# Kernel tuning notes

Hardware: AMD Instinct MI355X
Metric: run time of the kernel (lower is better)

## Reference

```python
import jax, jax.numpy as jnp
import numpy as np

ALPHA = 1.0
BETA = 0.25
NUM_EMBEDS = 8192
EMBED_DIM = 512
B, T = 32, 256


def setup_inputs() -> dict:
    key = jax.random.key(0)
    k1, k2 = jax.random.split(key)
    z_e = jax.random.normal(k1, (B, EMBED_DIM, T), dtype=jnp.float32)
    codebook = jax.random.normal(k2, (NUM_EMBEDS, EMBED_DIM), dtype=jnp.float32)
    return {"z_e": z_e, "codebook": codebook}


def reference(z_e, codebook):
    # z_e: (b, d, t) -> (b, t, d)
    z = jnp.transpose(z_e, (0, 2, 1))
    b, t, d = z.shape
    flat = z.reshape(-1, d)  # (N, d), N = b*t

    # squared euclidean distances to every codebook vector: (N, K)
    dists = (
        jnp.sum(flat * flat, axis=1, keepdims=True)
        + jnp.sum(codebook * codebook, axis=1)
        - 2.0 * flat @ codebook.T
    )
    idx = jnp.argmin(dists, axis=1)  # (N,)

    # codebook lookup (equivalent to one-hot @ codebook)
    z_q = codebook[idx].reshape(b, t, d)

    # commitment loss (codebook is EMA-updated, so only e_latent term)
    e_latent_loss = jnp.mean((jax.lax.stop_gradient(z_q) - z) ** 2)
    vq_loss = ALPHA * BETA * e_latent_loss

    # straight-through estimator
    z_q_st = z + jax.lax.stop_gradient(z_q - z)
    z_q_out = jnp.transpose(z_q_st, (0, 2, 1))  # back to (b, d, t)

    # perplexity from mean one-hot assignment probabilities
    counts = jnp.zeros((codebook.shape[0],), dtype=jnp.float32).at[idx].add(1.0)
    avg_probs = counts / flat.shape[0]
    perplexity = jnp.exp(-jnp.sum(avg_probs * jnp.log(avg_probs + 1e-10)))

    return z_q_out, vq_loss, perplexity
```

## Files before the change

kernel.cpp:

```cpp
#include <hip/hip_runtime.h>
#include <stdint.h>

typedef _Float16 half8 __attribute__((ext_vector_type(8)));
typedef float floatx16 __attribute__((ext_vector_type(16)));

#define ALPHA_ 1.0f
#define BETA_ 0.25f
#define NUM_EMBEDS 8192
#define EMBED_DIM 512
#define B_ 32
#define T_ 256
#define N_TOK 8192


typedef __attribute__((address_space(1))) const void ga_void;
typedef __attribute__((address_space(3))) void ls_void;
__device__ __forceinline__ void gl_lds16(const void* g, void* l) {
    __builtin_amdgcn_global_load_lds((ga_void*)g, (ls_void*)l, 16, 0, 0);
}

__global__ void pack_cb_kernel(const float* __restrict__ cb, _Float16* __restrict__ h,
                               _Float16* __restrict__ m, float* __restrict__ cnorm) {
    int row = blockIdx.x * 4 + (threadIdx.x >> 6);
    int lane = threadIdx.x & 63;
    const float* src = cb + (size_t)row * EMBED_DIM + lane * 8;
    float4 v0 = *(const float4*)src;
    float4 v1 = *(const float4*)(src + 4);
    float x[8] = {v0.x, v0.y, v0.z, v0.w, v1.x, v1.y, v1.z, v1.w};
    half8 hh, mm;
    float s = 0.f;
#pragma unroll
    for (int j = 0; j < 8; ++j) {
        s += x[j] * x[j];
        _Float16 hv = (_Float16)x[j];
        hh[j] = hv;
        mm[j] = (_Float16)((x[j] - (float)hv) * 2048.0f);
    }
    *(half8*)(h + (size_t)row * EMBED_DIM + lane * 8) = hh;
    *(half8*)(m + (size_t)row * EMBED_DIM + lane * 8) = mm;
#pragma unroll
    for (int d = 32; d; d >>= 1) s += __shfl_xor(s, d, 64);
    if (lane == 0) cnorm[row] = s;
}

__global__ void pack_z_kernel(const float* __restrict__ z, _Float16* __restrict__ h,
                              _Float16* __restrict__ m) {
    int tid = threadIdx.x;
    int lane = tid & 63, ds = tid >> 6;
    int b = blockIdx.x >> 2;
    int t = ((blockIdx.x & 3) << 6) + lane;
    size_t n = (size_t)b * T_ + t;
    for (int g = 0; g < 16; ++g) {
        int d0 = g * 32 + ds * 8;
        const float* src = z + ((size_t)b * EMBED_DIM + d0) * T_ + t;
        half8 hh, mm;
#pragma unroll
        for (int j = 0; j < 8; ++j) {
            float x = -2.0f * src[(size_t)j * T_];
            _Float16 hv = (_Float16)x;
            hh[j] = hv;
            mm[j] = (_Float16)((x - (float)hv) * 2048.0f);
        }
        *(half8*)(h + n * EMBED_DIM + d0) = hh;
        *(half8*)(m + n * EMBED_DIM + d0) = mm;
    }
}

__global__ __launch_bounds__(256, 2) void argmin_kernel(
    const _Float16* __restrict__ cb_h, const _Float16* __restrict__ cb_m,
    const _Float16* __restrict__ zt_h, const _Float16* __restrict__ zt_m,
    const float* __restrict__ cnorm, unsigned long long* __restrict__ wmin) {
    __shared__ _Float16 smem[8192];
    const int tid = threadIdx.x;
    const int lane = tid & 63;
    const int wv = tid >> 6;
    const int l31 = lane & 31;
    const int hf = lane >> 5;
    const int wp = wv >> 1, wq = wv & 1;
    const int n0 = blockIdx.x * 128;
    const int kbase = blockIdx.y * 1024;

    const _Float16* gplane = (wv == 0) ? cb_h : (wv == 1) ? cb_m : (wv == 2) ? zt_h : zt_m;
    const size_t gbase0 = ((wv < 2) ? (size_t)kbase : (size_t)n0) * EMBED_DIM +
                          (size_t)(lane >> 1) * EMBED_DIM + (size_t)(lane & 1) * 8;
    _Float16* lreg = &smem[wv * 2048];

    const int fro = l31 * 16 + hf * 8;

    unsigned long long best0 = ~0ULL, best1 = ~0ULL;

    for (int col = 0; col < 8; ++col) {
        const int kb = kbase + (col << 7);
        const _Float16* g = gplane + gbase0 + ((wv < 2) ? (size_t)(col << 7) * EMBED_DIM : 0);

        floatx16 acc1[2][2], acc2[2][2];
#pragma unroll
        for (int pi = 0; pi < 2; ++pi)
#pragma unroll
            for (int qi = 0; qi < 2; ++qi)
#pragma unroll
                for (int r = 0; r < 16; ++r) { acc1[pi][qi][r] = 0.f; acc2[pi][qi][r] = 0.f; }

#pragma unroll
        for (int i = 0; i < 4; ++i)
            gl_lds16(g + (size_t)(i * 32) * EMBED_DIM, lreg + i * 512);
        __syncthreads();

        for (int step = 0; step < 32; ++step) {
            half8 Ah[2], Am[2], Bh[2], Bm[2];
#pragma unroll
            for (int pi = 0; pi < 2; ++pi) {
                Ah[pi] = *(const half8*)&smem[(wp << 10) + (pi << 9) + fro];
                Am[pi] = *(const half8*)&smem[2048 + (wp << 10) + (pi << 9) + fro];
            }
#pragma unroll
            for (int qi = 0; qi < 2; ++qi) {
                Bh[qi] = *(const half8*)&smem[4096 + (wq << 10) + (qi << 9) + fro];
                Bm[qi] = *(const half8*)&smem[6144 + (wq << 10) + (qi << 9) + fro];
            }
            __syncthreads();
            if (step < 31) {
                const _Float16* gs = g + ((step + 1) << 4);
#pragma unroll
                for (int i = 0; i < 4; ++i)
                    gl_lds16(gs + (size_t)(i * 32) * EMBED_DIM, lreg + i * 512);
            }
#pragma unroll
            for (int pi = 0; pi < 2; ++pi)
#pragma unroll
                for (int qi = 0; qi < 2; ++qi) {
                    acc1[pi][qi] = __builtin_amdgcn_mfma_f32_32x32x16_f16(Ah[pi], Bh[qi], acc1[pi][qi], 0, 0, 0);
                    acc2[pi][qi] = __builtin_amdgcn_mfma_f32_32x32x16_f16(Ah[pi], Bm[qi], acc2[pi][qi], 0, 0, 0);
                    acc2[pi][qi] = __builtin_amdgcn_mfma_f32_32x32x16_f16(Am[pi], Bh[qi], acc2[pi][qi], 0, 0, 0);
                }
            __syncthreads();
        }

#pragma unroll
        for (int pi = 0; pi < 2; ++pi)
#pragma unroll
            for (int r = 0; r < 16; ++r) {
                int code = kb + (wp << 6) + (pi << 5) + (r & 3) + ((r >> 2) << 3) + (hf << 2);
                float cnv = cnorm[code];
                {
                    float s = cnv + acc1[pi][0][r] + acc2[pi][0][r] * (1.0f / 2048.0f);
                    uint32_t u = __float_as_uint(s);
                    u = (u & 0x80000000u) ? ~u : (u | 0x80000000u);
                    unsigned long long key = ((unsigned long long)u << 32) | (unsigned)code;
                    if (key < best0) best0 = key;
                }
                {
                    float s = cnv + acc1[pi][1][r] + acc2[pi][1][r] * (1.0f / 2048.0f);
                    uint32_t u = __float_as_uint(s);
                    u = (u & 0x80000000u) ? ~u : (u | 0x80000000u);
                    unsigned long long key = ((unsigned long long)u << 32) | (unsigned)code;
                    if (key < best1) best1 = key;
                }
            }
    }

    {
        unsigned long long o = __shfl_xor(best0, 32, 64);
        if (o < best0) best0 = o;
        o = __shfl_xor(best1, 32, 64);
        if (o < best1) best1 = o;
        if (hf == 0) {
            atomicMin(&wmin[n0 + (wq << 6) + l31], best0);
            atomicMin(&wmin[n0 + (wq << 6) + 32 + l31], best1);
        }
    }
}

__global__ void gather_kernel(const float* __restrict__ z, const float* __restrict__ cb,
                              const unsigned long long* __restrict__ wmin,
                              float* __restrict__ out, int* __restrict__ counts,
                              float* __restrict__ sse_acc) {
    __shared__ unsigned int sIdx[64];
    __shared__ float red[4];
    const int tid = threadIdx.x;
    const int n0 = blockIdx.x * 64;
    const int b = n0 >> 8;
    const int t0 = n0 & 255;
    if (tid < 64) {
        unsigned int idx = (unsigned int)(wmin[n0 + tid] & 0xffffffffULL);
        sIdx[tid] = idx;
        atomicAdd(&counts[idx], 1);
    }
    __syncthreads();
    const int w = tid >> 6;
    const int lane = tid & 63;
    const float* crow = cb + (size_t)sIdx[lane] * EMBED_DIM;
    const size_t base = ((size_t)b * EMBED_DIM) * T_ + (size_t)(t0 + lane);
    float sse = 0.f;
    for (int d = w; d < EMBED_DIM; d += 4) {
        float v = crow[d];
        size_t o = base + (size_t)d * T_;
        float diff = v - z[o];
        out[o] = v;
        sse += diff * diff;
    }
    for (int m = 32; m; m >>= 1) sse += __shfl_xor(sse, m, 64);
    if (lane == 0) red[w] = sse;
    __syncthreads();
    if (tid == 0) atomicAdd(sse_acc, red[0] + red[1] + red[2] + red[3]);
}

__global__ void finalize_kernel(const int* __restrict__ counts,
                                const float* __restrict__ sse_acc,
                                float* __restrict__ out) {
    __shared__ float red[4];
    const int tid = threadIdx.x;
    float e = 0.f;
    for (int k = tid; k < NUM_EMBEDS; k += 256) {
        float p = (float)counts[k] * (1.0f / (float)N_TOK);
        e += p * logf(p + 1e-10f);
    }
    for (int m = 32; m; m >>= 1) e += __shfl_xor(e, m, 64);
    if ((tid & 63) == 0) red[tid >> 6] = e;
    __syncthreads();
    if (tid == 0) {
        float ent = red[0] + red[1] + red[2] + red[3];
        size_t off = (size_t)B_ * EMBED_DIM * T_;
        out[off + 0] = (ALPHA_ * BETA_) * sse_acc[0] / (float)((size_t)N_TOK * EMBED_DIM);
        out[off + 1] = expf(-ent);
    }
}

extern "C" void kernel_launch(void* const* d_in, const int* in_sizes, int n_in,
                              void* d_out, int out_size, void* d_ws, size_t ws_size,
                              hipStream_t stream) {
    const float* z = (const float*)d_in[0];
    const float* cb = (const float*)d_in[1];
    float* out = (float*)d_out;
    char* ws = (char*)d_ws;
    unsigned long long* wmin = (unsigned long long*)ws;
    float* cnorm = (float*)(ws + 65536);
    int* counts = (int*)(ws + 98304);
    float* sse = (float*)(ws + 131072);
    _Float16* cb_h = (_Float16*)(ws + (1ull << 20));
    _Float16* cb_m = (_Float16*)(ws + (9ull << 20));
    _Float16* zt_h = (_Float16*)(ws + (17ull << 20));
    _Float16* zt_m = (_Float16*)(ws + (25ull << 20));

    hipMemsetAsync(wmin, 0xFF, NUM_EMBEDS * sizeof(unsigned long long), stream);
    hipMemsetAsync(counts, 0, NUM_EMBEDS * sizeof(int) + sizeof(float), stream);

    pack_cb_kernel<<<NUM_EMBEDS / 4, 256, 0, stream>>>(cb, cb_h, cb_m, cnorm);
    pack_z_kernel<<<(B_ * T_) / 64, 256, 0, stream>>>(z, zt_h, zt_m);
    argmin_kernel<<<dim3(N_TOK / 128, NUM_EMBEDS / 1024), 256, 0, stream>>>(cb_h, cb_m, zt_h, zt_m, cnorm, wmin);
    gather_kernel<<<N_TOK / 64, 256, 0, stream>>>(z, cb, wmin, out, counts, sse);
    finalize_kernel<<<1, 256, 0, stream>>>(counts, sse, out);
}
```

Baseline: 427.1 us.

## Interleave hi/lo fp16 planes, retile argmin to 128x128 tiles, add fp32 fallback for close calls

The hi and lo fp16 split planes are packed into one interleaved, XOR-swizzled row layout. The argmin is retiled so each block handles 128 tokens x 128 codes over the full depth, with double-buffered LDS stages of 64 elements. Each tile now records its best and second-best distance in per-slice slots instead of issuing atomicMin. A combine kernel reduces the 64 slices and sends tokens whose top-2 gap falls below a threshold to an exact fp32 fallback kernel. This is meant to cut synchronisation and improve MFMA-to-load overlap, at the cost of extra kernels and reliance on the gap threshold for correctness.

Result: faster. 363.3 us (-14.9%).

```diff
diff --git a/kernel.cpp b/kernel.cpp
--- a/kernel.cpp
+++ b/kernel.cpp
@@ -3,6 +3,7 @@
 
 typedef _Float16 half8 __attribute__((ext_vector_type(8)));
 typedef float floatx16 __attribute__((ext_vector_type(16)));
+typedef unsigned long long u64;
 
 #define ALPHA_ 1.0f
 #define BETA_ 0.25f
@@ -11,6 +12,7 @@
 #define B_ 32
 #define T_ 256
 #define N_TOK 8192
+#define THR_GAP 2e-3f
 
 
 typedef __attribute__((address_space(1))) const void ga_void;
@@ -19,8 +21,16 @@
     __builtin_amdgcn_global_load_lds((ga_void*)g, (ls_void*)l, 16, 0, 0);
 }
 
-__global__ void pack_cb_kernel(const float* __restrict__ cb, _Float16* __restrict__ h,
-                               _Float16* __restrict__ m, float* __restrict__ cnorm) {
+__device__ __forceinline__ uint32_t mono(float s) {
+    uint32_t u = __float_as_uint(s);
+    return (u & 0x80000000u) ? ~u : (u | 0x80000000u);
+}
+__device__ __forceinline__ float unmono(uint32_t v) {
+    return __uint_as_float((v & 0x80000000u) ? (v ^ 0x80000000u) : ~v);
+}
+
+__global__ void pack_cb_kernel(const float* __restrict__ cb, _Float16* __restrict__ ci,
+                               float* __restrict__ cnorm) {
     int row = blockIdx.x * 4 + (threadIdx.x >> 6);
     int lane = threadIdx.x & 63;
     const float* src = cb + (size_t)row * EMBED_DIM + lane * 8;
@@ -36,15 +46,15 @@
         hh[j] = hv;
         mm[j] = (_Float16)((x[j] - (float)hv) * 2048.0f);
     }
-    *(half8*)(h + (size_t)row * EMBED_DIM + lane * 8) = hh;
-    *(half8*)(m + (size_t)row * EMBED_DIM + lane * 8) = mm;
+    _Float16* dst = ci + (size_t)row * 1024 + lane * 16;
+    *(half8*)dst = hh;
+    *(half8*)(dst + 8) = mm;
 #pragma unroll
     for (int d = 32; d; d >>= 1) s += __shfl_xor(s, d, 64);
     if (lane == 0) cnorm[row] = s;
 }
 
-__global__ void pack_z_kernel(const float* __restrict__ z, _Float16* __restrict__ h,
-                              _Float16* __restrict__ m) {
+__global__ void pack_z_kernel(const float* __restrict__ z, _Float16* __restrict__ zi) {
     int tid = threadIdx.x;
     int lane = tid & 63, ds = tid >> 6;
     int b = blockIdx.x >> 2;
@@ -61,118 +71,195 @@
             hh[j] = hv;
             mm[j] = (_Float16)((x - (float)hv) * 2048.0f);
         }
-        *(half8*)(h + n * EMBED_DIM + d0) = hh;
-        *(half8*)(m + n * EMBED_DIM + d0) = mm;
-    }
-}
+        _Float16* dst = zi + n * 1024 + (size_t)(g * 4 + ds) * 16;
+        *(half8*)dst = hh;
+        *(half8*)(dst + 8) = mm;
+    }
+}
+
+#define MFMA16(a, b, c) __builtin_amdgcn_mfma_f32_32x32x16_f16(a, b, c, 0, 0, 0)
 
 __global__ __launch_bounds__(256, 2) void argmin_kernel(
-    const _Float16* __restrict__ cb_h, const _Float16* __restrict__ cb_m,
-    const _Float16* __restrict__ zt_h, const _Float16* __restrict__ zt_m,
-    const float* __restrict__ cnorm, unsigned long long* __restrict__ wmin) {
-    __shared__ _Float16 smem[8192];
+    const _Float16* __restrict__ cb_i, const _Float16* __restrict__ zt_i,
+    const float* __restrict__ cnorm, u64* __restrict__ slot_m1,
+    _Float16* __restrict__ slot_d) {
+    __shared__ _Float16 As[2][8192];
+    __shared__ _Float16 Bs[2][8192];
+    __shared__ u64 sK[128];
+    __shared__ float sV1[128], sV2[128];
     const int tid = threadIdx.x;
-    const int lane = tid & 63;
+    const int l = tid & 63;
     const int wv = tid >> 6;
-    const int l31 = lane & 31;
-    const int hf = lane >> 5;
+    const int l31 = l & 31;
+    const int hf = l >> 5;
     const int wp = wv >> 1, wq = wv & 1;
     const int n0 = blockIdx.x * 128;
-    const int kbase = blockIdx.y * 1024;
-
-    const _Float16* gplane = (wv == 0) ? cb_h : (wv == 1) ? cb_m : (wv == 2) ? zt_h : zt_m;
-    const size_t gbase0 = ((wv < 2) ? (size_t)kbase : (size_t)n0) * EMBED_DIM +
-                          (size_t)(lane >> 1) * EMBED_DIM + (size_t)(lane & 1) * 8;
-    _Float16* lreg = &smem[wv * 2048];
-
-    const int fro = l31 * 16 + hf * 8;
-
-    unsigned long long best0 = ~0ULL, best1 = ~0ULL;
-
-    for (int col = 0; col < 8; ++col) {
-        const int kb = kbase + (col << 7);
-        const _Float16* g = gplane + gbase0 + ((wv < 2) ? (size_t)(col << 7) * EMBED_DIM : 0);
-
-        floatx16 acc1[2][2], acc2[2][2];
-#pragma unroll
-        for (int pi = 0; pi < 2; ++pi)
-#pragma unroll
-            for (int qi = 0; qi < 2; ++qi)
-#pragma unroll
-                for (int r = 0; r < 16; ++r) { acc1[pi][qi][r] = 0.f; acc2[pi][qi][r] = 0.f; }
-
-#pragma unroll
-        for (int i = 0; i < 4; ++i)
-            gl_lds16(g + (size_t)(i * 32) * EMBED_DIM, lreg + i * 512);
+    const int c0 = blockIdx.y * 128;
+
+    const bool isA = wv < 2;
+    const _Float16* gsrc = isA ? cb_i : zt_i;
+    const int rbase = (isA ? c0 : n0) + ((wv & 1) << 6);
+    const int srow = l >> 3;
+    const int sseg = (l & 7) ^ srow;
+    const size_t lanefix = (size_t)(rbase + srow) * 1024 + sseg * 8;
+
+    floatx16 acc1[2][2], acc2[2][2];
+#pragma unroll
+    for (int a = 0; a < 2; ++a)
+#pragma unroll
+        for (int b = 0; b < 2; ++b)
+#pragma unroll
+            for (int r = 0; r < 16; ++r) { acc1[a][b][r] = 0.f; acc2[a][b][r] = 0.f; }
+
+    auto stage = [&](int p, int s) {
+        const _Float16* gs = gsrc + lanefix + (size_t)s * 64;
+        _Float16* lb = (isA ? As[p] : Bs[p]) + ((wv & 1) << 12);
+#pragma unroll
+        for (int j = 0; j < 8; ++j)
+            gl_lds16(gs + (size_t)j * 8192, lb + j * 512);
+    };
+
+    stage(0, 0);
+    __syncthreads();
+    for (int s = 0; s < 16; ++s) {
+        const int p = s & 1;
+        if (s < 15) stage(p ^ 1, s + 1);
+        const _Float16* Ab = As[p] + (wp * 64 + l31) * 64;
+        const _Float16* Bb = Bs[p] + (wq * 64 + l31) * 64;
+        const int rs = l31 & 7;
+#pragma unroll
+        for (int kk = 0; kk < 2; ++kk) {
+            const int j = kk * 2 + hf;
+            const int ph = ((2 * j) ^ rs) * 8;
+            const int pm = ((2 * j + 1) ^ rs) * 8;
+            half8 Ah0 = *(const half8*)(Ab + ph), Am0 = *(const half8*)(Ab + pm);
+            half8 Ah1 = *(const half8*)(Ab + 2048 + ph), Am1 = *(const half8*)(Ab + 2048 + pm);
+            half8 Bh0 = *(const half8*)(Bb + ph), Bm0 = *(const half8*)(Bb + pm);
+            half8 Bh1 = *(const half8*)(Bb + 2048 + ph), Bm1 = *(const half8*)(Bb + 2048 + pm);
+            acc1[0][0] = MFMA16(Ah0, Bh0, acc1[0][0]);
+            acc2[0][0] = MFMA16(Ah0, Bm0, acc2[0][0]);
+            acc2[0][0] = MFMA16(Am0, Bh0, acc2[0][0]);
+            acc1[0][1] = MFMA16(Ah0, Bh1, acc1[0][1]);
+            acc2[0][1] = MFMA16(Ah0, Bm1, acc2[0][1]);
+            acc2[0][1] = MFMA16(Am0, Bh1, acc2[0][1]);
+            acc1[1][0] = MFMA16(Ah1, Bh0, acc1[1][0]);
+            acc2[1][0] = MFMA16(Ah1, Bm0, acc2[1][0]);
+            acc2[1][0] = MFMA16(Am1, Bh0, acc2[1][0]);
+            acc1[1][1] = MFMA16(Ah1, Bh1, acc1[1][1]);
+            acc2[1][1] = MFMA16(Ah1, Bm1, acc2[1][1]);
+            acc2[1][1] = MFMA16(Am1, Bh1, acc2[1][1]);
+        }
         __syncthreads();
-
-        for (int step = 0; step < 32; ++step) {
-            half8 Ah[2], Am[2], Bh[2], Bm[2];
-#pragma unroll
-            for (int pi = 0; pi < 2; ++pi) {
-                Ah[pi] = *(const half8*)&smem[(wp << 10) + (pi << 9) + fro];
-                Am[pi] = *(const half8*)&smem[2048 + (wp << 10) + (pi << 9) + fro];
-            }
-#pragma unroll
-            for (int qi = 0; qi < 2; ++qi) {
-                Bh[qi] = *(const half8*)&smem[4096 + (wq << 10) + (qi << 9) + fro];
-                Bm[qi] = *(const half8*)&smem[6144 + (wq << 10) + (qi << 9) + fro];
-            }
-            __syncthreads();
-            if (step < 31) {
-                const _Float16* gs = g + ((step + 1) << 4);
-#pragma unroll
-                for (int i = 0; i < 4; ++i)
-                    gl_lds16(gs + (size_t)(i * 32) * EMBED_DIM, lreg + i * 512);
-            }
-#pragma unroll
-            for (int pi = 0; pi < 2; ++pi)
-#pragma unroll
-                for (int qi = 0; qi < 2; ++qi) {
-                    acc1[pi][qi] = __builtin_amdgcn_mfma_f32_32x32x16_f16(Ah[pi], Bh[qi], acc1[pi][qi], 0, 0, 0);
-                    acc2[pi][qi] = __builtin_amdgcn_mfma_f32_32x32x16_f16(Ah[pi], Bm[qi], acc2[pi][qi], 0, 0, 0);
-                    acc2[pi][qi] = __builtin_amdgcn_mfma_f32_32x32x16_f16(Am[pi], Bh[qi], acc2[pi][qi], 0, 0, 0);
-                }
-            __syncthreads();
-        }
-
-#pragma unroll
-        for (int pi = 0; pi < 2; ++pi)
-#pragma unroll
-            for (int r = 0; r < 16; ++r) {
-                int code = kb + (wp << 6) + (pi << 5) + (r & 3) + ((r >> 2) << 3) + (hf << 2);
-                float cnv = cnorm[code];
-                {
-                    float s = cnv + acc1[pi][0][r] + acc2[pi][0][r] * (1.0f / 2048.0f);
-                    uint32_t u = __float_as_uint(s);
-                    u = (u & 0x80000000u) ? ~u : (u | 0x80000000u);
-                    unsigned long long key = ((unsigned long long)u << 32) | (unsigned)code;
-                    if (key < best0) best0 = key;
-                }
-                {
-                    float s = cnv + acc1[pi][1][r] + acc2[pi][1][r] * (1.0f / 2048.0f);
-                    uint32_t u = __float_as_uint(s);
-                    u = (u & 0x80000000u) ? ~u : (u | 0x80000000u);
-                    unsigned long long key = ((unsigned long long)u << 32) | (unsigned)code;
-                    if (key < best1) best1 = key;
+    }
+
+    u64 km[2]; float kv1[2], kv2[2];
+#pragma unroll
+    for (int qi = 0; qi < 2; ++qi) {
+        u64 m1k = ~0ULL;
+        float m1v = 3.4e38f, m2 = 3.4e38f;
+#pragma unroll
+        for (int ti = 0; ti < 2; ++ti)
+#pragma unroll
+            for (int g = 0; g < 4; ++g) {
+                const int cb4 = c0 + wp * 64 + ti * 32 + g * 8 + hf * 4;
+                float4 cn = *(const float4*)(cnorm + cb4);
+                const floatx16& A1 = acc1[ti][qi];
+                const floatx16& A2 = acc2[ti][qi];
+                float sv[4] = {cn.x + A1[g * 4 + 0] + A2[g * 4 + 0] * (1.0f / 2048.0f),
+                               cn.y + A1[g * 4 + 1] + A2[g * 4 + 1] * (1.0f / 2048.0f),
+                               cn.z + A1[g * 4 + 2] + A2[g * 4 + 2] * (1.0f / 2048.0f),
+                               cn.w + A1[g * 4 + 3] + A2[g * 4 + 3] * (1.0f / 2048.0f)};
+#pragma unroll
+                for (int q = 0; q < 4; ++q) {
+                    u64 key = ((u64)mono(sv[q]) << 32) | (uint32_t)(cb4 + q);
+                    if (key < m1k) { m2 = m1v; m1v = sv[q]; m1k = key; }
+                    else m2 = fminf(m2, sv[q]);
                 }
             }
-    }
-
-    {
-        unsigned long long o = __shfl_xor(best0, 32, 64);
-        if (o < best0) best0 = o;
-        o = __shfl_xor(best1, 32, 64);
-        if (o < best1) best1 = o;
-        if (hf == 0) {
-            atomicMin(&wmin[n0 + (wq << 6) + l31], best0);
-            atomicMin(&wmin[n0 + (wq << 6) + 32 + l31], best1);
-        }
+        u64 ok = __shfl_xor(m1k, 32, 64);
+        float ov = __shfl_xor(m1v, 32, 64);
+        float om2 = __shfl_xor(m2, 32, 64);
+        if (ok < m1k) { m2 = fminf(fminf(m2, om2), m1v); m1v = ov; m1k = ok; }
+        else m2 = fminf(fminf(m2, om2), ov);
+        km[qi] = m1k; kv1[qi] = m1v; kv2[qi] = m2;
+    }
+    if (wp == 1 && hf == 0) {
+#pragma unroll
+        for (int qi = 0; qi < 2; ++qi) {
+            int idx = wq * 64 + qi * 32 + l31;
+            sK[idx] = km[qi]; sV1[idx] = kv1[qi]; sV2[idx] = kv2[qi];
+        }
+    }
+    __syncthreads();
+    if (wp == 0 && hf == 0) {
+#pragma unroll
+        for (int qi = 0; qi < 2; ++qi) {
+            int idx = wq * 64 + qi * 32 + l31;
+            u64 m1k = km[qi]; float m1v = kv1[qi], m2 = kv2[qi];
+            u64 ok = sK[idx]; float ov = sV1[idx], om2 = sV2[idx];
+            if (ok < m1k) { m2 = fminf(fminf(m2, om2), m1v); m1v = ov; m1k = ok; }
+            else m2 = fminf(fminf(m2, om2), ov);
+            int tok = n0 + idx;
+            slot_m1[((size_t)blockIdx.y << 13) + tok] = m1k;
+            slot_d[((size_t)blockIdx.y << 13) + tok] = (_Float16)(m2 - m1v);
+        }
+    }
+}
+
+__global__ void combine_kernel(const u64* __restrict__ slot_m1, const _Float16* __restrict__ slot_d,
+                               u64* __restrict__ wexact, int* __restrict__ worklist,
+                               int* __restrict__ nflag) {
+    int tok = blockIdx.x * 256 + threadIdx.x;
+    u64 g1 = ~0ULL;
+    float g1v = 3.4e38f, g2 = 3.4e38f;
+    for (int c = 0; c < 64; ++c) {
+        u64 k = slot_m1[((size_t)c << 13) + tok];
+        float kv = unmono((uint32_t)(k >> 32));
+        float v2 = kv + (float)slot_d[((size_t)c << 13) + tok];
+        if (k < g1) { g2 = fminf(g2, g1v); g1 = k; g1v = kv; }
+        else g2 = fminf(g2, kv);
+        g2 = fminf(g2, v2);
+    }
+    if (g2 - g1v > THR_GAP) wexact[tok] = g1;
+    else { int i = atomicAdd(nflag, 1); if (i < 8192) worklist[i] = tok; }
+}
+
+__global__ void fallback_kernel(const float* __restrict__ z, const float* __restrict__ cb,
+                                const float* __restrict__ cnorm,
+                                const int* __restrict__ worklist, const int* __restrict__ nflag,
+                                u64* __restrict__ wexact) {
+    int n = *nflag;
+    if (n > 8192) n = 8192;
+    const int l = threadIdx.x & 63, wv = threadIdx.x >> 6;
+    const int cbase = blockIdx.x * 128;
+    for (int fi = blockIdx.y; fi < n; fi += gridDim.y) {
+        int tok = worklist[fi];
+        int b = tok >> 8, t = tok & 255;
+        const float* zp = z + ((size_t)b * EMBED_DIM) * T_ + t;
+        float zr[8];
+#pragma unroll
+        for (int j = 0; j < 8; ++j) zr[j] = zp[(size_t)(l * 8 + j) * T_];
+        u64 m1 = ~0ULL;
+        for (int j = 0; j < 32; ++j) {
+            int c = cbase + wv + j * 4;
+            const float* cp = cb + (size_t)c * EMBED_DIM + l * 8;
+            float4 a = *(const float4*)cp, bb = *(const float4*)(cp + 4);
+            float dot = zr[0] * a.x + zr[1] * a.y + zr[2] * a.z + zr[3] * a.w +
+                        zr[4] * bb.x + zr[5] * bb.y + zr[6] * bb.z + zr[7] * bb.w;
+#pragma unroll
+            for (int m = 32; m; m >>= 1) dot += __shfl_xor(dot, m, 64);
+            if (l == 0) {
+                float s = cnorm[c] - 2.0f * dot;
+                u64 key = ((u64)mono(s) << 32) | (uint32_t)c;
+                if (key < m1) m1 = key;
+            }
+        }
+        if (l == 0) atomicMin(&wexact[tok], m1);
     }
 }
 
 __global__ void gather_kernel(const float* __restrict__ z, const float* __restrict__ cb,
-                              const unsigned long long* __restrict__ wmin,
+                              const u64* __restrict__ wexact,
                               float* __restrict__ out, int* __restrict__ counts,
                               float* __restrict__ sse_acc) {
     __shared__ unsigned int sIdx[64];
@@ -182,7 +269,7 @@
     const int b = n0 >> 8;
     const int t0 = n0 & 255;
     if (tid < 64) {
-        unsigned int idx = (unsigned int)(wmin[n0 + tid] & 0xffffffffULL);
+        unsigned int idx = (unsigned int)(wexact[n0 + tid] & 0xffffffffULL);
         sIdx[tid] = idx;
         atomicAdd(&counts[idx], 1);
     }
@@ -233,21 +320,25 @@
     const float* cb = (const float*)d_in[1];
     float* out = (float*)d_out;
     char* ws = (char*)d_ws;
-    unsigned long long* wmin = (unsigned long long*)ws;
+    u64* wexact = (u64*)ws;
     float* cnorm = (float*)(ws + 65536);
     int* counts = (int*)(ws + 98304);
     float* sse = (float*)(ws + 131072);
-    _Float16* cb_h = (_Float16*)(ws + (1ull << 20));
-    _Float16* cb_m = (_Float16*)(ws + (9ull << 20));
-    _Float16* zt_h = (_Float16*)(ws + (17ull << 20));
-    _Float16* zt_m = (_Float16*)(ws + (25ull << 20));
-
-    hipMemsetAsync(wmin, 0xFF, NUM_EMBEDS * sizeof(unsigned long long), stream);
-    hipMemsetAsync(counts, 0, NUM_EMBEDS * sizeof(int) + sizeof(float), stream);
-
-    pack_cb_kernel<<<NUM_EMBEDS / 4, 256, 0, stream>>>(cb, cb_h, cb_m, cnorm);
-    pack_z_kernel<<<(B_ * T_) / 64, 256, 0, stream>>>(z, zt_h, zt_m);
-    argmin_kernel<<<dim3(N_TOK / 128, NUM_EMBEDS / 1024), 256, 0, stream>>>(cb_h, cb_m, zt_h, zt_m, cnorm, wmin);
-    gather_kernel<<<N_TOK / 64, 256, 0, stream>>>(z, cb, wmin, out, counts, sse);
+    int* nflag = (int*)(ws + 131076);
+    int* worklist = (int*)(ws + 131080);
+    u64* slot_m1 = (u64*)(ws + (1ull << 20));
+    _Float16* slot_d = (_Float16*)(ws + (5ull << 20));
+    _Float16* cb_i = (_Float16*)(ws + (6ull << 20));
+    _Float16* zt_i = (_Float16*)(ws + (22ull << 20));
+
+    hipMemsetAsync(wexact, 0xFF, NUM_EMBEDS * sizeof(u64), stream);
+    hipMemsetAsync(counts, 0, NUM_EMBEDS * sizeof(int) + 8, stream);
+
+    pack_cb_kernel<<<NUM_EMBEDS / 4, 256, 0, stream>>>(cb, cb_i, cnorm);
+    pack_z_kernel<<<N_TOK / 64, 256, 0, stream>>>(z, zt_i);
+    argmin_kernel<<<dim3(N_TOK / 128, NUM_EMBEDS / 128), 256, 0, stream>>>(cb_i, zt_i, cnorm, slot_m1, slot_d);
+    combine_kernel<<<N_TOK / 256, 256, 0, stream>>>(slot_m1, slot_d, wexact, worklist, nflag);
+    fallback_kernel<<<dim3(64, 16), 256, 0, stream>>>(z, cb, cnorm, worklist, nflag, wexact);
+    gather_kernel<<<N_TOK / 64, 256, 0, stream>>>(z, cb, wexact, out, counts, sse);
     finalize_kernel<<<1, 256, 0, stream>>>(counts, sse, out);
 }
```
